# Performance work log

Hardware: AMD Instinct MI355X
Metric: run time of the kernel (lower is better)

The kernel has to match this reference:

```python
import jax, jax.numpy as jnp
from jax import lax
import numpy as np

T, B, H, I, O = 2048, 256, 512, 1, 1


def setup_inputs() -> dict:
    key = jax.random.key(0)
    k = jax.random.split(key, 7)
    scale = 1.0 / np.sqrt(H)  # pytorch uniform init bound
    u = lambda kk, sh: jax.random.uniform(kk, sh, jnp.float32, -scale, scale)
    return {
        "input_seq": jax.random.normal(k[0], (T, B), jnp.float32),
        "W_ih": u(k[1], (4 * H, I)),   # gate order: i, f, g, o
        "W_hh": u(k[2], (4 * H, H)),
        "b_ih": u(k[3], (4 * H,)),
        "b_hh": u(k[4], (4 * H,)),
        "W_lin": u(k[5], (O, H)),
        "b_lin": u(k[6], (O,)),
    }


def reference(input_seq, W_ih, W_hh, b_ih, b_hh, W_lin, b_lin):
    # input_seq: [T, B] -> unsqueeze to [T, B, 1]
    x = input_seq[:, :, None]
    # precompute input projection for all timesteps: [T, B, 4H]
    x_proj = jnp.einsum('tbi,gi->tbg', x, W_ih) + (b_ih + b_hh)

    h0 = jnp.zeros((B, H), input_seq.dtype)
    c0 = jnp.zeros((B, H), input_seq.dtype)

    def step(carry, xp):
        h, c = carry
        gates = xp + h @ W_hh.T  # [B, 4H]
        i, f, g, o = jnp.split(gates, 4, axis=-1)
        i = jax.nn.sigmoid(i)
        f = jax.nn.sigmoid(f)
        g = jnp.tanh(g)
        o = jax.nn.sigmoid(o)
        c = f * c + i * g
        h = o * jnp.tanh(c)
        return (h, c), None

    (h_last, _), _ = lax.scan(step, (h0, c0), x_proj)
    # linear head on last timestep's hidden state: [B, O]
    return h_last @ W_lin.T + b_lin
```

## Files before the change

### kernel.cpp

```cpp
#include <hip/hip_runtime.h>

#define T_STEPS 2048
#define BATCH   256
#define HID     512
#define NG      16
#define NB      16
#define RING    6
#define SENT    0x3C3C3C3C

typedef _Float16 half8 __attribute__((ext_vector_type(8)));
typedef float f32x4 __attribute__((ext_vector_type(4)));
typedef int int4v __attribute__((ext_vector_type(4)));

__device__ __forceinline__ float sigmoid_f(float v) {
    return 1.f / (1.f + __expf(-v));
}
__device__ __forceinline__ float tanh_f(float v) {
    float a = fabsf(v);
    float e = __expf(2.f * a);
    float r = 1.f - 2.f / (e + 1.f);
    return copysignf(r, v);
}

__global__ __launch_bounds__(256, 1) void lstm_persistent(
    const float* __restrict__ x,
    const float* __restrict__ Wih,
    const float* __restrict__ Whh,
    const float* __restrict__ bih,
    const float* __restrict__ bhh,
    const float* __restrict__ Wlin,
    _Float16* __restrict__ hbuf,
    float* __restrict__ partial)
{
    const int tid  = threadIdx.x;
    const int g    = blockIdx.x & 15;
    const int j    = blockIdx.x >> 4;
    const int wave = tid >> 6;
    const int lane = tid & 63;
    const int quad = lane >> 4;
    const int ln16 = lane & 15;

    __shared__ float lds_part[2][4][4][16][34];

    half8 bf[4][2][4];
    #pragma unroll
    for (int gt = 0; gt < 4; ++gt) {
        #pragma unroll
        for (int ch = 0; ch < 2; ++ch) {
            const float* wr = Whh + (size_t)(gt * 512 + j * 32 + ch * 16 + ln16) * HID;
            #pragma unroll
            for (int ksl = 0; ksl < 4; ++ksl) {
                int k0 = (wave * 4 + ksl) * 32 + quad * 8;
                half8 v;
                #pragma unroll
                for (int e = 0; e < 8; ++e) v[e] = (_Float16)wr[k0 + e];
                bf[gt][ch][ksl] = v;
            }
        }
    }

    const int row_e = tid >> 4;
    const int cp    = (tid & 15) * 2;

    float wxA[4], wxB[4], bsA[4], bsB[4];
    #pragma unroll
    for (int gt = 0; gt < 4; ++gt) {
        int r0 = gt * 512 + j * 32 + cp;
        wxA[gt] = Wih[r0];
        wxB[gt] = Wih[r0 + 1];
        bsA[gt] = bih[r0] + bhh[r0];
        bsB[gt] = bih[r0 + 1] + bhh[r0 + 1];
    }

    float c0 = 0.f, c1 = 0.f;
    float hl0 = 0.f, hl1 = 0.f;
    bool  dead = false;

    float x_cur = x[(size_t)g * 16 + row_e];

    int s_in = 0, s_out = 1, s_rst = 5;

    for (int t = 0; t < T_STEPS; ++t) {
        unsigned long long haddr = (unsigned long long)(
            (const char*)hbuf
            + ((size_t)s_in * (BATCH * HID) + (size_t)(g * 16 + ln16) * HID) * 2
            + wave * 256 + quad * 16);
        int4v h0, h1, h2, h3;
        {
            unsigned it = 0;
            for (;;) {
                asm volatile(
                    "global_load_dwordx4 %0, %4, off sc0 sc1\n\t"
                    "global_load_dwordx4 %1, %4, off offset:64 sc0 sc1\n\t"
                    "global_load_dwordx4 %2, %4, off offset:128 sc0 sc1\n\t"
                    "global_load_dwordx4 %3, %4, off offset:192 sc0 sc1\n\t"
                    "s_waitcnt vmcnt(0)"
                    : "=&v"(h0), "=&v"(h1), "=&v"(h2), "=&v"(h3)
                    : "v"(haddr) : "memory");
                bool ok = true;
                #pragma unroll
                for (int e = 0; e < 4; ++e) {
                    ok = ok && (h0[e] != (int)SENT) && (h1[e] != (int)SENT)
                            && (h2[e] != (int)SENT) && (h3[e] != (int)SENT);
                }
                if (__ballot(ok) == ~0ull || dead) break;
                if (++it > 100000000u) { dead = true; break; }
            }
        }

        float x_next = x[(size_t)(t + 1 < T_STEPS ? t + 1 : t) * BATCH + g * 16 + row_e];

        f32x4 acc[4][2];
        #pragma unroll
        for (int gt = 0; gt < 4; ++gt) {
            acc[gt][0] = (f32x4){0.f, 0.f, 0.f, 0.f};
            acc[gt][1] = (f32x4){0.f, 0.f, 0.f, 0.f};
        }
        #define KSTEP(ksl, hx) {                                                      \
            half8 af = __builtin_bit_cast(half8, hx);                                 \
            _Pragma("unroll")                                                         \
            for (int gt = 0; gt < 4; ++gt) {                                          \
                acc[gt][0] = __builtin_amdgcn_mfma_f32_16x16x32_f16(af, bf[gt][0][ksl], acc[gt][0], 0, 0, 0); \
                acc[gt][1] = __builtin_amdgcn_mfma_f32_16x16x32_f16(af, bf[gt][1][ksl], acc[gt][1], 0, 0, 0); \
            } }
        KSTEP(0, h0) KSTEP(1, h1) KSTEP(2, h2) KSTEP(3, h3)
        #undef KSTEP

        const int tb = t & 1;
        #pragma unroll
        for (int gt = 0; gt < 4; ++gt) {
            #pragma unroll
            for (int r = 0; r < 4; ++r) {
                lds_part[tb][wave][gt][quad * 4 + r][ln16]      = acc[gt][0][r];
                lds_part[tb][wave][gt][quad * 4 + r][16 + ln16] = acc[gt][1][r];
            }
        }
        __syncthreads();

        {
            unsigned long long radr = (unsigned long long)(
                (char*)hbuf
                + ((size_t)s_rst * (BATCH * HID)
                   + (size_t)(g * 16 + row_e) * HID + j * 32 + cp) * 2);
            unsigned sv = SENT;
            asm volatile("global_store_dword %0, %1, off sc0 sc1"
                         : : "v"(radr), "v"(sv) : "memory");
        }

        const float xin = x_cur;
        float sA[4] = {0.f, 0.f, 0.f, 0.f};
        float sB[4] = {0.f, 0.f, 0.f, 0.f};
        #pragma unroll
        for (int w = 0; w < 4; ++w) {
            #pragma unroll
            for (int gt = 0; gt < 4; ++gt) {
                float2 v = *(const float2*)&lds_part[tb][w][gt][row_e][cp];
                sA[gt] += v.x;
                sB[gt] += v.y;
            }
        }
        float hv0, hv1;
        {
            float gi = sA[0] + xin * wxA[0] + bsA[0];
            float gf = sA[1] + xin * wxA[1] + bsA[1];
            float gg = sA[2] + xin * wxA[2] + bsA[2];
            float go = sA[3] + xin * wxA[3] + bsA[3];
            float iv = sigmoid_f(gi), fv = sigmoid_f(gf), gv = tanh_f(gg), ov = sigmoid_f(go);
            c0 = fv * c0 + iv * gv;
            hv0 = ov * tanh_f(c0);
        }
        {
            float gi = sB[0] + xin * wxB[0] + bsB[0];
            float gf = sB[1] + xin * wxB[1] + bsB[1];
            float gg = sB[2] + xin * wxB[2] + bsB[2];
            float go = sB[3] + xin * wxB[3] + bsB[3];
            float iv = sigmoid_f(gi), fv = sigmoid_f(gf), gv = tanh_f(gg), ov = sigmoid_f(go);
            c1 = fv * c1 + iv * gv;
            hv1 = ov * tanh_f(c1);
        }
        hl0 = hv0; hl1 = hv1;

        {
            _Float16 p0 = (_Float16)hv0, p1 = (_Float16)hv1;
            unsigned hbits = ((unsigned)__builtin_bit_cast(unsigned short, p1) << 16)
                           |  (unsigned)__builtin_bit_cast(unsigned short, p0);
            unsigned long long sadr = (unsigned long long)(
                (char*)hbuf
                + ((size_t)s_out * (BATCH * HID)
                   + (size_t)(g * 16 + row_e) * HID + j * 32 + cp) * 2);
            asm volatile("global_store_dword %0, %1, off sc0 sc1"
                         : : "v"(sadr), "v"(hbits) : "memory");
        }
        asm volatile("s_waitcnt vmcnt(0)" ::: "memory");

        x_cur = x_next;
        s_rst = s_in;
        s_in  = s_out;
        s_out = (s_out + 1 == RING) ? 0 : s_out + 1;
    }

    float p = hl0 * Wlin[j * 32 + cp] + hl1 * Wlin[j * 32 + cp + 1];
    #pragma unroll
    for (int off = 8; off; off >>= 1) p += __shfl_down(p, off, 16);
    if ((tid & 15) == 0) partial[(size_t)j * BATCH + g * 16 + row_e] = p;
}

__global__ void lstm_finalize(const float* __restrict__ partial,
                              const float* __restrict__ blin,
                              float* __restrict__ out)
{
    int b = threadIdx.x;
    float s = blin[0];
    #pragma unroll
    for (int jj = 0; jj < NG; ++jj) s += partial[(size_t)jj * BATCH + b];
    out[b] = s;
}

extern "C" void kernel_launch(void* const* d_in, const int* in_sizes, int n_in,
                              void* d_out, int out_size, void* d_ws, size_t ws_size,
                              hipStream_t stream) {
    const float* x    = (const float*)d_in[0];
    const float* Wih  = (const float*)d_in[1];
    const float* Whh  = (const float*)d_in[2];
    const float* bih  = (const float*)d_in[3];
    const float* bhh  = (const float*)d_in[4];
    const float* Wlin = (const float*)d_in[5];
    const float* blin = (const float*)d_in[6];

    char* ws = (char*)d_ws;
    _Float16* hbuf    = (_Float16*)ws;
    float*    partial = (float*)(ws + (2 << 20));

    const size_t slot_bytes = (size_t)BATCH * HID * sizeof(_Float16);
    hipMemsetAsync(hbuf, 0, slot_bytes, stream);
    hipMemsetAsync((char*)hbuf + slot_bytes, 0x3C, (RING - 1) * slot_bytes, stream);

    lstm_persistent<<<dim3(256), dim3(256), 0, stream>>>(
        x, Wih, Whh, bih, bhh, Wlin, hbuf, partial);
    lstm_finalize<<<dim3(1), dim3(256), 0, stream>>>(partial, blin, (float*)d_out);
}
```

Baseline: 4.545 ms.

## Consolidate batch tiles into 64 persistent blocks processing four sub-tiles serially

The persistent LSTM kernel drops from 256 to 64 blocks. Each block now loops over four 16-row batch sub-tiles per timestep, keeping cell state, last hidden state and x per sub-tile, and the trailing vmcnt wait at the end of each step is removed. The aim is to cut the number of blocks taking part in the cross-block spin-wait handshake and to overlap one sub-tile's polling latency with work on the other sub-tiles. The cost is four times more serial MFMA, LDS and activation work per block per step, on a quarter of the compute units.

```diff
diff --git a/kernel.cpp b/kernel.cpp
--- a/kernel.cpp
+++ b/kernel.cpp
@@ -4,7 +4,8 @@
 #define BATCH   256
 #define HID     512
 #define NG      16
-#define NB      16
+#define NSG     4
+#define NST     4
 #define RING    6
 #define SENT    0x3C3C3C3C
 
@@ -33,8 +34,8 @@
     float* __restrict__ partial)
 {
     const int tid  = threadIdx.x;
-    const int g    = blockIdx.x & 15;
-    const int j    = blockIdx.x >> 4;
+    const int sg   = blockIdx.x & 3;
+    const int j    = blockIdx.x >> 2;
     const int wave = tid >> 6;
     const int lane = tid & 63;
     const int quad = lane >> 4;
@@ -72,137 +73,147 @@
         bsB[gt] = bih[r0 + 1] + bhh[r0 + 1];
     }
 
-    float c0 = 0.f, c1 = 0.f;
-    float hl0 = 0.f, hl1 = 0.f;
-    bool  dead = false;
-
-    float x_cur = x[(size_t)g * 16 + row_e];
+    float c0[NST], c1[NST], hl0[NST], hl1[NST], x_cur[NST];
+    #pragma unroll
+    for (int st = 0; st < NST; ++st) {
+        c0[st] = 0.f; c1[st] = 0.f; hl0[st] = 0.f; hl1[st] = 0.f;
+        x_cur[st] = x[(size_t)(sg * 64 + st * 16 + row_e)];
+    }
+    bool dead = false;
 
     int s_in = 0, s_out = 1, s_rst = 5;
 
     for (int t = 0; t < T_STEPS; ++t) {
-        unsigned long long haddr = (unsigned long long)(
-            (const char*)hbuf
-            + ((size_t)s_in * (BATCH * HID) + (size_t)(g * 16 + ln16) * HID) * 2
-            + wave * 256 + quad * 16);
-        int4v h0, h1, h2, h3;
-        {
-            unsigned it = 0;
-            for (;;) {
-                asm volatile(
-                    "global_load_dwordx4 %0, %4, off sc0 sc1\n\t"
-                    "global_load_dwordx4 %1, %4, off offset:64 sc0 sc1\n\t"
-                    "global_load_dwordx4 %2, %4, off offset:128 sc0 sc1\n\t"
-                    "global_load_dwordx4 %3, %4, off offset:192 sc0 sc1\n\t"
-                    "s_waitcnt vmcnt(0)"
-                    : "=&v"(h0), "=&v"(h1), "=&v"(h2), "=&v"(h3)
-                    : "v"(haddr) : "memory");
-                bool ok = true;
+        #pragma unroll
+        for (int st = 0; st < NST; ++st) {
+            const int row_base = sg * 64 + st * 16;
+            const int pb = st & 1;
+
+            unsigned long long haddr = (unsigned long long)(
+                (const char*)hbuf
+                + ((size_t)s_in * (BATCH * HID) + (size_t)(row_base + ln16) * HID) * 2
+                + wave * 256 + quad * 16);
+            int4v h0, h1, h2, h3;
+            {
+                unsigned it = 0;
+                for (;;) {
+                    asm volatile(
+                        "global_load_dwordx4 %0, %4, off sc0 sc1\n\t"
+                        "global_load_dwordx4 %1, %4, off offset:64 sc0 sc1\n\t"
+                        "global_load_dwordx4 %2, %4, off offset:128 sc0 sc1\n\t"
+                        "global_load_dwordx4 %3, %4, off offset:192 sc0 sc1\n\t"
+                        "s_waitcnt vmcnt(0)"
+                        : "=&v"(h0), "=&v"(h1), "=&v"(h2), "=&v"(h3)
+                        : "v"(haddr) : "memory");
+                    bool ok = true;
+                    #pragma unroll
+                    for (int e = 0; e < 4; ++e) {
+                        ok = ok && (h0[e] != (int)SENT) && (h1[e] != (int)SENT)
+                                && (h2[e] != (int)SENT) && (h3[e] != (int)SENT);
+                    }
+                    if (__ballot(ok) == ~0ull || dead) break;
+                    if (++it > 100000000u) { dead = true; break; }
+                }
+            }
+
+            float x_next = x[(size_t)(t + 1 < T_STEPS ? t + 1 : t) * BATCH + row_base + row_e];
+
+            f32x4 acc[4][2];
+            #pragma unroll
+            for (int gt = 0; gt < 4; ++gt) {
+                acc[gt][0] = (f32x4){0.f, 0.f, 0.f, 0.f};
+                acc[gt][1] = (f32x4){0.f, 0.f, 0.f, 0.f};
+            }
+            #define KSTEP(ksl, hx) {                                                      \
+                half8 af = __builtin_bit_cast(half8, hx);                                 \
+                _Pragma("unroll")                                                         \
+                for (int gt = 0; gt < 4; ++gt) {                                          \
+                    acc[gt][0] = __builtin_amdgcn_mfma_f32_16x16x32_f16(af, bf[gt][0][ksl], acc[gt][0], 0, 0, 0); \
+                    acc[gt][1] = __builtin_amdgcn_mfma_f32_16x16x32_f16(af, bf[gt][1][ksl], acc[gt][1], 0, 0, 0); \
+                } }
+            KSTEP(0, h0) KSTEP(1, h1) KSTEP(2, h2) KSTEP(3, h3)
+            #undef KSTEP
+
+            #pragma unroll
+            for (int gt = 0; gt < 4; ++gt) {
                 #pragma unroll
-                for (int e = 0; e < 4; ++e) {
-                    ok = ok && (h0[e] != (int)SENT) && (h1[e] != (int)SENT)
-                            && (h2[e] != (int)SENT) && (h3[e] != (int)SENT);
+                for (int r = 0; r < 4; ++r) {
+                    lds_part[pb][wave][gt][quad * 4 + r][ln16]      = acc[gt][0][r];
+                    lds_part[pb][wave][gt][quad * 4 + r][16 + ln16] = acc[gt][1][r];
                 }
-                if (__ballot(ok) == ~0ull || dead) break;
-                if (++it > 100000000u) { dead = true; break; }
-            }
+            }
+            __syncthreads();
+
+            {
+                unsigned long long radr = (unsigned long long)(
+                    (char*)hbuf
+                    + ((size_t)s_rst * (BATCH * HID)
+                       + (size_t)(row_base + row_e) * HID + j * 32 + cp) * 2);
+                unsigned sv = SENT;
+                asm volatile("global_store_dword %0, %1, off sc0 sc1"
+                             : : "v"(radr), "v"(sv) : "memory");
+            }
+
+            const float xin = x_cur[st];
+            float sA[4] = {0.f, 0.f, 0.f, 0.f};
+            float sB[4] = {0.f, 0.f, 0.f, 0.f};
+            #pragma unroll
+            for (int w = 0; w < 4; ++w) {
+                #pragma unroll
+                for (int gt = 0; gt < 4; ++gt) {
+                    float2 v = *(const float2*)&lds_part[pb][w][gt][row_e][cp];
+                    sA[gt] += v.x;
+                    sB[gt] += v.y;
+                }
+            }
+            float hv0, hv1;
+            {
+                float gi = sA[0] + xin * wxA[0] + bsA[0];
+                float gf = sA[1] + xin * wxA[1] + bsA[1];
+                float gg = sA[2] + xin * wxA[2] + bsA[2];
+                float go = sA[3] + xin * wxA[3] + bsA[3];
+                float iv = sigmoid_f(gi), fv = sigmoid_f(gf), gv = tanh_f(gg), ov = sigmoid_f(go);
+                c0[st] = fv * c0[st] + iv * gv;
+                hv0 = ov * tanh_f(c0[st]);
+            }
+            {
+                float gi = sB[0] + xin * wxB[0] + bsB[0];
+                float gf = sB[1] + xin * wxB[1] + bsB[1];
+                float gg = sB[2] + xin * wxB[2] + bsB[2];
+                float go = sB[3] + xin * wxB[3] + bsB[3];
+                float iv = sigmoid_f(gi), fv = sigmoid_f(gf), gv = tanh_f(gg), ov = sigmoid_f(go);
+                c1[st] = fv * c1[st] + iv * gv;
+                hv1 = ov * tanh_f(c1[st]);
+            }
+            hl0[st] = hv0; hl1[st] = hv1;
+
+            {
+                _Float16 p0 = (_Float16)hv0, p1 = (_Float16)hv1;
+                unsigned hbits = ((unsigned)__builtin_bit_cast(unsigned short, p1) << 16)
+                               |  (unsigned)__builtin_bit_cast(unsigned short, p0);
+                unsigned long long sadr = (unsigned long long)(
+                    (char*)hbuf
+                    + ((size_t)s_out * (BATCH * HID)
+                       + (size_t)(row_base + row_e) * HID + j * 32 + cp) * 2);
+                asm volatile("global_store_dword %0, %1, off sc0 sc1"
+                             : : "v"(sadr), "v"(hbits) : "memory");
+            }
+            x_cur[st] = x_next;
         }
 
-        float x_next = x[(size_t)(t + 1 < T_STEPS ? t + 1 : t) * BATCH + g * 16 + row_e];
-
-        f32x4 acc[4][2];
-        #pragma unroll
-        for (int gt = 0; gt < 4; ++gt) {
-            acc[gt][0] = (f32x4){0.f, 0.f, 0.f, 0.f};
-            acc[gt][1] = (f32x4){0.f, 0.f, 0.f, 0.f};
-        }
-        #define KSTEP(ksl, hx) {                                                      \
-            half8 af = __builtin_bit_cast(half8, hx);                                 \
-            _Pragma("unroll")                                                         \
-            for (int gt = 0; gt < 4; ++gt) {                                          \
-                acc[gt][0] = __builtin_amdgcn_mfma_f32_16x16x32_f16(af, bf[gt][0][ksl], acc[gt][0], 0, 0, 0); \
-                acc[gt][1] = __builtin_amdgcn_mfma_f32_16x16x32_f16(af, bf[gt][1][ksl], acc[gt][1], 0, 0, 0); \
-            } }
-        KSTEP(0, h0) KSTEP(1, h1) KSTEP(2, h2) KSTEP(3, h3)
-        #undef KSTEP
-
-        const int tb = t & 1;
-        #pragma unroll
-        for (int gt = 0; gt < 4; ++gt) {
-            #pragma unroll
-            for (int r = 0; r < 4; ++r) {
-                lds_part[tb][wave][gt][quad * 4 + r][ln16]      = acc[gt][0][r];
-                lds_part[tb][wave][gt][quad * 4 + r][16 + ln16] = acc[gt][1][r];
-            }
-        }
-        __syncthreads();
-
-        {
-            unsigned long long radr = (unsigned long long)(
-                (char*)hbuf
-                + ((size_t)s_rst * (BATCH * HID)
-                   + (size_t)(g * 16 + row_e) * HID + j * 32 + cp) * 2);
-            unsigned sv = SENT;
-            asm volatile("global_store_dword %0, %1, off sc0 sc1"
-                         : : "v"(radr), "v"(sv) : "memory");
-        }
-
-        const float xin = x_cur;
-        float sA[4] = {0.f, 0.f, 0.f, 0.f};
-        float sB[4] = {0.f, 0.f, 0.f, 0.f};
-        #pragma unroll
-        for (int w = 0; w < 4; ++w) {
-            #pragma unroll
-            for (int gt = 0; gt < 4; ++gt) {
-                float2 v = *(const float2*)&lds_part[tb][w][gt][row_e][cp];
-                sA[gt] += v.x;
-                sB[gt] += v.y;
-            }
-        }
-        float hv0, hv1;
-        {
-            float gi = sA[0] + xin * wxA[0] + bsA[0];
-            float gf = sA[1] + xin * wxA[1] + bsA[1];
-            float gg = sA[2] + xin * wxA[2] + bsA[2];
-            float go = sA[3] + xin * wxA[3] + bsA[3];
-            float iv = sigmoid_f(gi), fv = sigmoid_f(gf), gv = tanh_f(gg), ov = sigmoid_f(go);
-            c0 = fv * c0 + iv * gv;
-            hv0 = ov * tanh_f(c0);
-        }
-        {
-            float gi = sB[0] + xin * wxB[0] + bsB[0];
-            float gf = sB[1] + xin * wxB[1] + bsB[1];
-            float gg = sB[2] + xin * wxB[2] + bsB[2];
-            float go = sB[3] + xin * wxB[3] + bsB[3];
-            float iv = sigmoid_f(gi), fv = sigmoid_f(gf), gv = tanh_f(gg), ov = sigmoid_f(go);
-            c1 = fv * c1 + iv * gv;
-            hv1 = ov * tanh_f(c1);
-        }
-        hl0 = hv0; hl1 = hv1;
-
-        {
-            _Float16 p0 = (_Float16)hv0, p1 = (_Float16)hv1;
-            unsigned hbits = ((unsigned)__builtin_bit_cast(unsigned short, p1) << 16)
-                           |  (unsigned)__builtin_bit_cast(unsigned short, p0);
-            unsigned long long sadr = (unsigned long long)(
-                (char*)hbuf
-                + ((size_t)s_out * (BATCH * HID)
-                   + (size_t)(g * 16 + row_e) * HID + j * 32 + cp) * 2);
-            asm volatile("global_store_dword %0, %1, off sc0 sc1"
-                         : : "v"(sadr), "v"(hbits) : "memory");
-        }
-        asm volatile("s_waitcnt vmcnt(0)" ::: "memory");
-
-        x_cur = x_next;
         s_rst = s_in;
         s_in  = s_out;
         s_out = (s_out + 1 == RING) ? 0 : s_out + 1;
     }
 
-    float p = hl0 * Wlin[j * 32 + cp] + hl1 * Wlin[j * 32 + cp + 1];
-    #pragma unroll
-    for (int off = 8; off; off >>= 1) p += __shfl_down(p, off, 16);
-    if ((tid & 15) == 0) partial[(size_t)j * BATCH + g * 16 + row_e] = p;
+    #pragma unroll
+    for (int st = 0; st < NST; ++st) {
+        float p = hl0[st] * Wlin[j * 32 + cp] + hl1[st] * Wlin[j * 32 + cp + 1];
+        #pragma unroll
+        for (int off = 8; off; off >>= 1) p += __shfl_down(p, off, 16);
+        if ((tid & 15) == 0)
+            partial[(size_t)j * BATCH + sg * 64 + st * 16 + row_e] = p;
+    }
 }
 
 __global__ void lstm_finalize(const float* __restrict__ partial,
@@ -235,7 +246,7 @@
     hipMemsetAsync(hbuf, 0, slot_bytes, stream);
     hipMemsetAsync((char*)hbuf + slot_bytes, 0x3C, (RING - 1) * slot_bytes, stream);
 
-    lstm_persistent<<<dim3(256), dim3(256), 0, stream>>>(
+    lstm_persistent<<<dim3(64), dim3(256), 0, stream>>>(
         x, Wih, Whh, bih, bhh, Wlin, hbuf, partial);
     lstm_finalize<<<dim3(1), dim3(256), 0, stream>>>(partial, blin, (float*)d_out);
 }
```

Measured after the change: 15.47 ms. +240.3%, slower.
